# Kernel tuning notes

Hardware: AMD Instinct MI355X
Metric: run time of the kernel (lower is better)

## Reference

```python
import jax, jax.numpy as jnp
import numpy as np

N_NODES = 50000
N_EDGES = 1600000
IN_CH = 128
HID_CH = 128


def setup_inputs() -> dict:
    key = jax.random.key(0)
    ks = jax.random.split(key, 8)
    node_embed = jax.random.normal(ks[0], (N_NODES, IN_CH), dtype=jnp.float32)
    node_pos = jax.random.normal(ks[1], (N_NODES, 3), dtype=jnp.float32)
    edge_index = jax.random.randint(ks[2], (2, N_EDGES), 0, N_NODES, dtype=jnp.int64)
    # Linear weights stored as [in, out] so y = x @ W + b (matches torch x @ W.T + b)
    W_res = jax.random.normal(ks[3], (IN_CH, HID_CH), dtype=jnp.float32) / np.sqrt(IN_CH)
    W_msg = jax.random.normal(ks[4], (2 * IN_CH + 1, HID_CH), dtype=jnp.float32) / np.sqrt(2 * IN_CH + 1)
    b_msg = jax.random.normal(ks[5], (HID_CH,), dtype=jnp.float32) * 0.01
    W_upd = jax.random.normal(ks[6], (IN_CH + HID_CH, HID_CH), dtype=jnp.float32) / np.sqrt(IN_CH + HID_CH)
    b_upd = jax.random.normal(ks[7], (HID_CH,), dtype=jnp.float32) * 0.01
    return {"node_embed": node_embed, "node_pos": node_pos, "edge_index": edge_index,
            "W_res": W_res, "W_msg": W_msg, "b_msg": b_msg, "W_upd": W_upd, "b_upd": b_upd}


def reference(node_embed, node_pos, edge_index, W_res, W_msg, b_msg, W_upd, b_upd):
    row, col = edge_index[0], edge_index[1]
    # squared distance per edge: [E, 1]
    diff = node_pos[row] - node_pos[col]
    dist = jnp.sum(diff * diff, axis=1, keepdims=True)
    # message MLP on concat(src, tgt, dist): [E, 2*in+1] -> [E, hidden]
    msg_in = jnp.concatenate([node_embed[row], node_embed[col], dist], axis=-1)
    msg = jax.nn.relu(msg_in @ W_msg + b_msg)
    # scatter-sum messages into target nodes (index = col, as in original)
    aggr = jax.ops.segment_sum(msg, col, num_segments=N_NODES)
    upd_in = jnp.concatenate([node_embed, aggr], axis=-1)
    new_node_embed = node_embed @ W_res + jax.nn.relu(upd_in @ W_upd + b_upd)
    return new_node_embed
```

## Files before the change

kernel.cpp:

```cpp
#include <hip/hip_runtime.h>
#include <hip/hip_bf16.h>
#include <cstdint>


typedef __bf16 bf16x8 __attribute__((ext_vector_type(8)));
typedef float floatx4 __attribute__((ext_vector_type(4)));
typedef float floatx2 __attribute__((ext_vector_type(2)));
typedef unsigned int uintx4 __attribute__((ext_vector_type(4)));

#define NBINS 1024
#define NCPY 8
#define BINF_CAP 384
#define CAP_OUT 2816
#define CUR_STRIDE 32
#define EPB 8192

__device__ __forceinline__ ushort f2bf(float f) {
  union { float f; uint i; } v; v.f = f;
  uint r = v.i + 0x7fff + ((v.i >> 16) & 1);
  return (ushort)(r >> 16);
}
__device__ __forceinline__ bf16x8 load_frag(const ushort* p) {
  uint4 v = *(const uint4*)p;
  return __builtin_bit_cast(bf16x8, v);
}
__device__ __forceinline__ floatx2 pmax0(floatx2 a) {
#if __has_builtin(__builtin_elementwise_max)
  return __builtin_elementwise_max(a, (floatx2)(0.f));
#else
  floatx2 r; r.x = fmaxf(a.x, 0.f); r.y = fmaxf(a.y, 0.f); return r;
#endif
}
__device__ __forceinline__ floatx2 cvtpk2(uint qu) {
#if __has_builtin(__builtin_amdgcn_cvt_pk_f32_fp8)
  return __builtin_amdgcn_cvt_pk_f32_fp8((int)qu, false);
#else
  floatx2 o = {__builtin_amdgcn_cvt_f32_fp8((int)qu, 0),
               __builtin_amdgcn_cvt_f32_fp8((int)qu, 1)};
  return o;
#endif
}

struct WSrc { const float* s[5]; };

__global__ __launch_bounds__(256) void k01_cast_bin(
    const float* __restrict__ embed, ushort* __restrict__ Eb, int n4, int nb_cast,
    WSrc ws, ushort* __restrict__ Wt,
    const int* __restrict__ ei, int E,
    uint* __restrict__ bin_cursor, uint* __restrict__ binned, int bb)
{
  __shared__ uint hist[NBINS];
  __shared__ uint sbase[NBINS];
  __shared__ uint lcur[NBINS];

  if ((int)blockIdx.x >= bb) {
    int cb = blockIdx.x - bb;
    if (cb < nb_cast) {
      int base = cb * 2048 + threadIdx.x;
#pragma unroll
      for (int k = 0; k < 8; ++k) {
        int i = base + k * 256;
        if (i < n4) {
          float4 v = ((const float4*)embed)[i];
          ushort4 o;
          o.x = f2bf(v.x); o.y = f2bf(v.y); o.z = f2bf(v.z); o.w = f2bf(v.w);
          ((ushort4*)Eb)[i] = o;
        }
      }
      return;
    }
    int wb = cb - nb_cast;
    const float* s = ws.s[wb];
    ushort* d = Wt + wb * 16384;
    for (int i = threadIdx.x; i < 16384; i += 256) {
      int k = i >> 7, n = i & 127;
      d[n * 128 + k] = f2bf(s[i]);
    }
    return;
  }

  const int t = threadIdx.x;
#pragma unroll
  for (int k = 0; k < NBINS / 256; ++k) hist[t + k * 256] = 0;
  __syncthreads();

  const int blk0 = blockIdx.x * EPB;
#pragma unroll
  for (int c = 0; c < EPB / 2048; ++c) {
    int e0 = blk0 + c * 2048 + t * 8;
    if (e0 < E) {
      int4 c0 = ((const int4*)(ei + E + e0))[0];
      int4 c1 = ((const int4*)(ei + E + e0))[1];
      int cc[8];
      cc[0]=c0.x; cc[1]=c0.y; cc[2]=c0.z; cc[3]=c0.w;
      cc[4]=c1.x; cc[5]=c1.y; cc[6]=c1.z; cc[7]=c1.w;
#pragma unroll
      for (int j = 0; j < 8; ++j)
        if (e0 + j < E) atomicAdd(&hist[cc[j] >> 6], 1u);
    }
  }
  __syncthreads();

  const int cpy = blockIdx.x & 7;
  uint* cur = bin_cursor + (size_t)cpy * NBINS * CUR_STRIDE;
#pragma unroll
  for (int k = 0; k < NBINS / 256; ++k) {
    int b2 = t + k * 256;
    uint h = hist[b2];
    sbase[b2] = h ? atomicAdd(cur + (size_t)b2 * CUR_STRIDE, h) : 0u;
    lcur[b2] = 0;
  }
  __syncthreads();

  uint* mybin = binned + (size_t)cpy * NBINS * BINF_CAP;
#pragma unroll
  for (int c = 0; c < EPB / 2048; ++c) {
    int e0 = blk0 + c * 2048 + t * 8;
    if (e0 < E) {
      int4 r0 = ((const int4*)(ei + e0))[0];
      int4 r1 = ((const int4*)(ei + e0))[1];
      int4 c0 = ((const int4*)(ei + E + e0))[0];
      int4 c1 = ((const int4*)(ei + E + e0))[1];
      int rr[8], cc[8];
      rr[0]=r0.x; rr[1]=r0.y; rr[2]=r0.z; rr[3]=r0.w;
      rr[4]=r1.x; rr[5]=r1.y; rr[6]=r1.z; rr[7]=r1.w;
      cc[0]=c0.x; cc[1]=c0.y; cc[2]=c0.z; cc[3]=c0.w;
      cc[4]=c1.x; cc[5]=c1.y; cc[6]=c1.z; cc[7]=c1.w;
#pragma unroll
      for (int j = 0; j < 8; ++j) {
        if (e0 + j < E) {
          int b = cc[j] >> 6;
          uint ofs = atomicAdd(&lcur[b], 1u);
          uint idx = sbase[b] + ofs;
          if (idx < BINF_CAP)
            mybin[(size_t)b * BINF_CAP + idx] = ((uint)cc[j] << 16) | (uint)rr[j];
        }
      }
    }
  }
}

__global__ __launch_bounds__(256) void k2_proj_sort(
    const ushort* __restrict__ Ab, int M, int rt,
    const ushort* __restrict__ W1t, const ushort* __restrict__ W2t,
    const float* __restrict__ b_msg, const float* __restrict__ pos,
    unsigned char* __restrict__ P1, ushort* __restrict__ P2b,
    const uint* __restrict__ bin_cursor, const uint* __restrict__ binned,
    uint* __restrict__ sorted, int* __restrict__ nstart, int* __restrict__ ncnt)
{
  __shared__ ushort sdist[NCPY * BINF_CAP];
  __shared__ uint   srt[CAP_OUT];
  __shared__ float  spos[64 * 3];
  __shared__ uint   h64[64], st64[64], lc64[64];
  __shared__ uint   ccnt[NCPY];
  __shared__ uint   stot;

  if ((int)blockIdx.x >= rt) {
    const int bin = blockIdx.x - rt;
    const int col0 = bin * 64;
    const int ncol = min(64, M - col0);
    const int tid = threadIdx.x;

    if (tid < 64) { h64[tid] = 0; lc64[tid] = 0; }
    if (tid < NCPY)
      ccnt[tid] = min(bin_cursor[((size_t)tid * NBINS + bin) * CUR_STRIDE],
                      (uint)BINF_CAP);
    for (int i = tid; i < ncol * 3; i += 256) spos[i] = pos[(size_t)col0 * 3 + i];
    __syncthreads();

    for (int c = 0; c < NCPY; ++c) {
      const int cnt = (int)ccnt[c];
      const uint* src = binned + ((size_t)c * NBINS + bin) * BINF_CAP;
      for (int i = tid; i < cnt; i += 256) {
        uint rc = src[i];
        uint row = rc & 0xffffu, c6 = (rc >> 16) & 63u;
        float dx = spos[c6 * 3 + 0] - pos[(size_t)row * 3 + 0];
        float dy = spos[c6 * 3 + 1] - pos[(size_t)row * 3 + 1];
        float dz = spos[c6 * 3 + 2] - pos[(size_t)row * 3 + 2];
        sdist[c * BINF_CAP + i] = f2bf(dx * dx + dy * dy + dz * dz);
        atomicAdd(&h64[c6], 1u);
      }
    }
    __syncthreads();

    if (tid == 0) {
      uint run = 0;
      for (int c = 0; c < 64; ++c) { st64[c] = run; run += (h64[c] + 3u) & ~3u; }
      stot = min(run, (uint)CAP_OUT);
    }
    __syncthreads();

    for (int c = 0; c < NCPY; ++c) {
      const int cnt = (int)ccnt[c];
      const uint* src = binned + ((size_t)c * NBINS + bin) * BINF_CAP;
      for (int i = tid; i < cnt; i += 256) {
        uint rc = src[i];
        uint c6 = (rc >> 16) & 63u;
        uint p = st64[c6] + atomicAdd(&lc64[c6], 1u);
        if (p < CAP_OUT)
          srt[p] = ((rc & 0xffffu) << 16) | (uint)sdist[c * BINF_CAP + i];
      }
    }
    __syncthreads();

    const size_t obase = (size_t)bin * CAP_OUT;
    for (int i = tid; i < (int)stot; i += 256)
      sorted[obase + i] = srt[i];
    if (tid < ncol) {
      nstart[col0 + tid] = (int)(obase + st64[tid]);
      ncnt[col0 + tid] = (int)h64[tid];
    }
    return;
  }

  const int wv = threadIdx.x >> 6, lane = threadIdx.x & 63;
  const int q = lane >> 4, lr = lane & 15;
  const int m0 = blockIdx.x * 32;
  const int n0 = wv * 32;

  const ushort* Wt2[2] = {W1t, W2t};
  bf16x8 bfr[2][2][4];
#pragma unroll
  for (int ws = 0; ws < 2; ++ws)
#pragma unroll
    for (int nt = 0; nt < 2; ++nt) {
      int colc = n0 + nt * 16 + lr;
#pragma unroll
      for (int kc = 0; kc < 4; ++kc)
        bfr[ws][nt][kc] = load_frag(Wt2[ws] + colc * 128 + kc * 32 + q * 8);
    }

  floatx4 z = {0.f, 0.f, 0.f, 0.f};
  floatx4 acc[2][2][2];
#pragma unroll
  for (int ws = 0; ws < 2; ++ws)
#pragma unroll
    for (int mt = 0; mt < 2; ++mt)
#pragma unroll
      for (int nt = 0; nt < 2; ++nt) acc[ws][mt][nt] = z;

  const int r0 = min(m0 + lr, M - 1);
  const int r1 = min(m0 + 16 + lr, M - 1);
#pragma unroll
  for (int kc = 0; kc < 4; ++kc) {
    bf16x8 a0 = load_frag(Ab + (size_t)r0 * 128 + kc * 32 + q * 8);
    bf16x8 a1 = load_frag(Ab + (size_t)r1 * 128 + kc * 32 + q * 8);
#pragma unroll
    for (int ws = 0; ws < 2; ++ws)
#pragma unroll
      for (int nt = 0; nt < 2; ++nt) {
        acc[ws][0][nt] = __builtin_amdgcn_mfma_f32_16x16x32_bf16(a0, bfr[ws][nt][kc], acc[ws][0][nt], 0, 0, 0);
        acc[ws][1][nt] = __builtin_amdgcn_mfma_f32_16x16x32_bf16(a1, bfr[ws][nt][kc], acc[ws][1][nt], 0, 0, 0);
      }
  }

#pragma unroll
  for (int nt = 0; nt < 2; ++nt) {
    int colc = n0 + nt * 16 + lr;
    float bias = b_msg[colc];
#pragma unroll
    for (int mt = 0; mt < 2; ++mt)
#pragma unroll
      for (int i = 0; i < 4; ++i) {
        int r = m0 + mt * 16 + q * 4 + i;
        if (r < M) {
          int p8 = __builtin_amdgcn_cvt_pk_fp8_f32(acc[0][mt][nt][i], 0.f, 0, false);
          P1[(size_t)r * 128 + colc] = (unsigned char)(p8 & 0xff);
          P2b[(size_t)r * 128 + colc] = f2bf(acc[1][mt][nt][i] + bias);
        }
      }
  }
}

__global__ __launch_bounds__(256) void aggregate(const int* __restrict__ ncnt,
                                                 const int* __restrict__ nstart,
                                                 const uint* __restrict__ sorted,
                                                 const unsigned char* __restrict__ P1,
                                                 const ushort* __restrict__ P2b,
                                                 const float* __restrict__ wd,
                                                 ushort* __restrict__ aggr, int M)
{
  const int lane = threadIdx.x & 63;
  const int ch = lane * 2;
  const int wid = blockIdx.x * 4 + (threadIdx.x >> 6);
  const int nw = gridDim.x * 4;

  float2 wl = *(const float2*)(wd + ch);
  floatx2 wv = {wl.x, wl.y};

  for (int n = wid; n < M; n += nw) {
    uint p2u = *(const uint*)(P2b + (size_t)n * 128 + ch);
    floatx2 p2 = {__int_as_float((int)(p2u << 16)),
                  __int_as_float((int)(p2u & 0xffff0000u))};

    const int cnt = ncnt[n];
    const uint* base = sorted + nstart[n];

    floatx2 accA = {0.f, 0.f}, accB = {0.f, 0.f};

    auto edge = [&](uint rec, floatx2& acc) {
      float d = __int_as_float((int)(rec << 16));
      uint off = ((rec >> 9) & 0x007fff80u) | (uint)ch;
      uint qu = (uint)*(const ushort*)(P1 + off);
#if __has_builtin(__builtin_elementwise_fma)
      floatx2 u = __builtin_elementwise_fma((floatx2)(d), wv, p2);
#else
      floatx2 u = (floatx2)(d) * wv + p2;
#endif
      floatx2 t = cvtpk2(qu) + u;
      acc += pmax0(t);
    };

    int i = 0;
    for (; i + 8 <= cnt; i += 8) {
      uintx4 ra = __builtin_nontemporal_load((const uintx4*)(base + i));
      uintx4 rb = __builtin_nontemporal_load((const uintx4*)(base + i + 4));
      edge(ra.x, accA); edge(ra.y, accB); edge(ra.z, accA); edge(ra.w, accB);
      edge(rb.x, accA); edge(rb.y, accB); edge(rb.z, accA); edge(rb.w, accB);
    }
    for (; i < cnt; ++i) edge(base[i], accA);

    floatx2 acc = accA + accB;
    uint o = (uint)f2bf(acc.x) | ((uint)f2bf(acc.y) << 16);
    *(uint*)(aggr + (size_t)n * 128 + ch) = o;
  }
}

__global__ __launch_bounds__(256) void gemm_upd_mfma(
    const ushort* __restrict__ Eb, const ushort* __restrict__ Gb, int M,
    const ushort* __restrict__ Wu1t, const ushort* __restrict__ Wu2t,
    const ushort* __restrict__ Wrt, const float* __restrict__ b_upd,
    float* __restrict__ out)
{
  const int wv = threadIdx.x >> 6, lane = threadIdx.x & 63;
  const int q = lane >> 4, lr = lane & 15;
  const int m0 = blockIdx.x * 128;
  const int n0 = wv * 32;

  bf16x8 b1[2][4], b2[2][4], br[2][4];
#pragma unroll
  for (int nt = 0; nt < 2; ++nt) {
    int colc = n0 + nt * 16 + lr;
#pragma unroll
    for (int kc = 0; kc < 4; ++kc) {
      b1[nt][kc] = load_frag(Wu1t + colc * 128 + kc * 32 + q * 8);
      b2[nt][kc] = load_frag(Wu2t + colc * 128 + kc * 32 + q * 8);
      br[nt][kc] = load_frag(Wrt  + colc * 128 + kc * 32 + q * 8);
    }
  }

  floatx4 z = {0.f, 0.f, 0.f, 0.f};

  for (int rc = 0; rc < 4; ++rc) {
    const int mb = m0 + rc * 32;
    if (mb >= M) break;

    floatx4 acc_u[2][2], acc_r[2][2];
#pragma unroll
    for (int mt = 0; mt < 2; ++mt)
#pragma unroll
      for (int nt = 0; nt < 2; ++nt) { acc_u[mt][nt] = z; acc_r[mt][nt] = z; }

    const int r0 = min(mb + lr, M - 1);
    const int r1 = min(mb + 16 + lr, M - 1);
#pragma unroll
    for (int kc = 0; kc < 4; ++kc) {
      bf16x8 ae0 = load_frag(Eb + (size_t)r0 * 128 + kc * 32 + q * 8);
      bf16x8 ae1 = load_frag(Eb + (size_t)r1 * 128 + kc * 32 + q * 8);
      bf16x8 ag0 = load_frag(Gb + (size_t)r0 * 128 + kc * 32 + q * 8);
      bf16x8 ag1 = load_frag(Gb + (size_t)r1 * 128 + kc * 32 + q * 8);
#pragma unroll
      for (int nt = 0; nt < 2; ++nt) {
        acc_u[0][nt] = __builtin_amdgcn_mfma_f32_16x16x32_bf16(ae0, b1[nt][kc], acc_u[0][nt], 0, 0, 0);
        acc_u[1][nt] = __builtin_amdgcn_mfma_f32_16x16x32_bf16(ae1, b1[nt][kc], acc_u[1][nt], 0, 0, 0);
        acc_u[0][nt] = __builtin_amdgcn_mfma_f32_16x16x32_bf16(ag0, b2[nt][kc], acc_u[0][nt], 0, 0, 0);
        acc_u[1][nt] = __builtin_amdgcn_mfma_f32_16x16x32_bf16(ag1, b2[nt][kc], acc_u[1][nt], 0, 0, 0);
        acc_r[0][nt] = __builtin_amdgcn_mfma_f32_16x16x32_bf16(ae0, br[nt][kc], acc_r[0][nt], 0, 0, 0);
        acc_r[1][nt] = __builtin_amdgcn_mfma_f32_16x16x32_bf16(ae1, br[nt][kc], acc_r[1][nt], 0, 0, 0);
      }
    }

#pragma unroll
    for (int nt = 0; nt < 2; ++nt) {
      int colc = n0 + nt * 16 + lr;
      float bias = b_upd[colc];
#pragma unroll
      for (int mt = 0; mt < 2; ++mt)
#pragma unroll
        for (int i = 0; i < 4; ++i) {
          int r = mb + mt * 16 + q * 4 + i;
          if (r < M)
            out[(size_t)r * 128 + colc] = acc_r[mt][nt][i] + fmaxf(acc_u[mt][nt][i] + bias, 0.f);
        }
    }
  }
}

extern "C" void kernel_launch(void* const* d_in, const int* in_sizes, int n_in,
                              void* d_out, int out_size, void* d_ws, size_t ws_size,
                              hipStream_t stream)
{
  const float* embed = (const float*)d_in[0];
  const float* pos   = (const float*)d_in[1];
  const int*   ei    = (const int*)d_in[2];
  const float* W_res = (const float*)d_in[3];
  const float* W_msg = (const float*)d_in[4];
  const float* b_msg = (const float*)d_in[5];
  const float* W_upd = (const float*)d_in[6];
  const float* b_upd = (const float*)d_in[7];
  float* out = (float*)d_out;

  const int M = in_sizes[0] / 128;
  const int E = in_sizes[2] / 2;

  ushort* Eb = (ushort*)d_ws;
  unsigned char* P1f8 = (unsigned char*)(Eb + (size_t)M * 128);
  ushort* P2b = (ushort*)(P1f8 + (size_t)M * 128);
  ushort* Gb  = P2b + (size_t)M * 128;
  ushort* Wt  = Gb  + (size_t)M * 128;
  uint*   binned = (uint*)(Wt + 5 * 16384);
  uint*   sorted = binned + (size_t)NCPY * NBINS * BINF_CAP;
  int*    nstart = (int*)(sorted + (size_t)NBINS * CAP_OUT);
  int*    ncnt   = nstart + M;
  uint*   bin_cursor = (uint*)(ncnt + M);

  (void)hipMemsetAsync(bin_cursor, 0,
                       (size_t)NCPY * NBINS * CUR_STRIDE * sizeof(uint), stream);

  WSrc wsrc;
  wsrc.s[0] = W_msg;
  wsrc.s[1] = W_msg + 128 * 128;
  wsrc.s[2] = W_res;
  wsrc.s[3] = W_upd;
  wsrc.s[4] = W_upd + 128 * 128;

  int n4 = M * 128 / 4;
  int nb_cast = (n4 + 2047) / 2048;
  int bb = (E + EPB - 1) / EPB;
  k01_cast_bin<<<bb + nb_cast + 5, 256, 0, stream>>>(
      embed, Eb, n4, nb_cast, wsrc, Wt, ei, E, bin_cursor, binned, bb);

  int rt = (M + 31) / 32;
  int nb2 = (M + 63) / 64;
  k2_proj_sort<<<rt + nb2, 256, 0, stream>>>(
      Eb, M, rt, Wt, Wt + 16384, b_msg, pos, P1f8, P2b,
      bin_cursor, binned, sorted, nstart, ncnt);

  int ab = min((M + 3) / 4, 2048);
  aggregate<<<ab, 256, 0, stream>>>(ncnt, nstart, sorted, P1f8, P2b,
                                    W_msg + 256 * 128, Gb, M);

  int rt4 = (M + 127) / 128;
  gemm_upd_mfma<<<rt4, 256, 0, stream>>>(Eb, Gb, M, Wt + 3 * 16384, Wt + 4 * 16384,
                                         Wt + 2 * 16384, b_upd, out);
}
```

Before: 227.9 us.

## Hoist embed-only update and residual GEMMs into projection/sort kernel

Moves the node_embed@W_upd[:128] (with bias) and node_embed@W_res products out of the final kernel and into k2_proj_sort as extra blocks, storing them as bf16 U and R buffers. The final kernel then only does the aggregate GEMM and adds U and R from memory. The aim is to cut the serial tail after aggregation and overlap those GEMMs with the binning/sort blocks. In exchange, U and R add global write and read traffic, and R is now rounded to bf16, which costs some precision.

```diff
diff --git a/kernel.cpp b/kernel.cpp
--- a/kernel.cpp
+++ b/kernel.cpp
@@ -19,6 +19,9 @@
   union { float f; uint i; } v; v.f = f;
   uint r = v.i + 0x7fff + ((v.i >> 16) & 1);
   return (ushort)(r >> 16);
+}
+__device__ __forceinline__ float bf2f(ushort u) {
+  return __int_as_float((int)((uint)u << 16));
 }
 __device__ __forceinline__ bf16x8 load_frag(const ushort* p) {
   uint4 v = *(const uint4*)p;
@@ -141,12 +144,15 @@
 }
 
 __global__ __launch_bounds__(256) void k2_proj_sort(
-    const ushort* __restrict__ Ab, int M, int rt,
+    const ushort* __restrict__ Ab, int M, int rt, int nsrt,
     const ushort* __restrict__ W1t, const ushort* __restrict__ W2t,
-    const float* __restrict__ b_msg, const float* __restrict__ pos,
+    const ushort* __restrict__ Wu1t, const ushort* __restrict__ Wrt,
+    const float* __restrict__ b_msg, const float* __restrict__ b_upd,
+    const float* __restrict__ pos,
     unsigned char* __restrict__ P1, ushort* __restrict__ P2b,
     const uint* __restrict__ bin_cursor, const uint* __restrict__ binned,
-    uint* __restrict__ sorted, int* __restrict__ nstart, int* __restrict__ ncnt)
+    uint* __restrict__ sorted, int* __restrict__ nstart, int* __restrict__ ncnt,
+    ushort* __restrict__ U, ushort* __restrict__ R)
 {
   __shared__ ushort sdist[NCPY * BINF_CAP];
   __shared__ uint   srt[CAP_OUT];
@@ -155,8 +161,9 @@
   __shared__ uint   ccnt[NCPY];
   __shared__ uint   stot;
 
-  if ((int)blockIdx.x >= rt) {
-    const int bin = blockIdx.x - rt;
+  const int bid = (int)blockIdx.x;
+  if (bid >= rt && bid < rt + nsrt) {
+    const int bin = bid - rt;
     const int col0 = bin * 64;
     const int ncol = min(64, M - col0);
     const int tid = threadIdx.x;
@@ -213,12 +220,16 @@
     return;
   }
 
+  const bool up = (bid >= rt);
+  const int m0 = (up ? (bid - rt - nsrt) : bid) * 32;
   const int wv = threadIdx.x >> 6, lane = threadIdx.x & 63;
   const int q = lane >> 4, lr = lane & 15;
-  const int m0 = blockIdx.x * 32;
   const int n0 = wv * 32;
 
-  const ushort* Wt2[2] = {W1t, W2t};
+  const ushort* Wt2[2];
+  if (up) { Wt2[0] = Wu1t; Wt2[1] = Wrt; }
+  else    { Wt2[0] = W1t;  Wt2[1] = W2t; }
+
   bf16x8 bfr[2][2][4];
 #pragma unroll
   for (int ws = 0; ws < 2; ++ws)
@@ -254,21 +265,39 @@
       }
   }
 
-#pragma unroll
-  for (int nt = 0; nt < 2; ++nt) {
-    int colc = n0 + nt * 16 + lr;
-    float bias = b_msg[colc];
-#pragma unroll
-    for (int mt = 0; mt < 2; ++mt)
-#pragma unroll
-      for (int i = 0; i < 4; ++i) {
-        int r = m0 + mt * 16 + q * 4 + i;
-        if (r < M) {
-          int p8 = __builtin_amdgcn_cvt_pk_fp8_f32(acc[0][mt][nt][i], 0.f, 0, false);
-          P1[(size_t)r * 128 + colc] = (unsigned char)(p8 & 0xff);
-          P2b[(size_t)r * 128 + colc] = f2bf(acc[1][mt][nt][i] + bias);
+  if (up) {
+#pragma unroll
+    for (int nt = 0; nt < 2; ++nt) {
+      int colc = n0 + nt * 16 + lr;
+      float bias = b_upd[colc];
+#pragma unroll
+      for (int mt = 0; mt < 2; ++mt)
+#pragma unroll
+        for (int i = 0; i < 4; ++i) {
+          int r = m0 + mt * 16 + q * 4 + i;
+          if (r < M) {
+            U[(size_t)r * 128 + colc] = f2bf(acc[0][mt][nt][i] + bias);
+            R[(size_t)r * 128 + colc] = f2bf(acc[1][mt][nt][i]);
+          }
         }
-      }
+    }
+  } else {
+#pragma unroll
+    for (int nt = 0; nt < 2; ++nt) {
+      int colc = n0 + nt * 16 + lr;
+      float bias = b_msg[colc];
+#pragma unroll
+      for (int mt = 0; mt < 2; ++mt)
+#pragma unroll
+        for (int i = 0; i < 4; ++i) {
+          int r = m0 + mt * 16 + q * 4 + i;
+          if (r < M) {
+            int p8 = __builtin_amdgcn_cvt_pk_fp8_f32(acc[0][mt][nt][i], 0.f, 0, false);
+            P1[(size_t)r * 128 + colc] = (unsigned char)(p8 & 0xff);
+            P2b[(size_t)r * 128 + colc] = f2bf(acc[1][mt][nt][i] + bias);
+          }
+        }
+    }
   }
 }
 
@@ -326,71 +355,63 @@
   }
 }
 
-__global__ __launch_bounds__(256) void gemm_upd_mfma(
-    const ushort* __restrict__ Eb, const ushort* __restrict__ Gb, int M,
-    const ushort* __restrict__ Wu1t, const ushort* __restrict__ Wu2t,
-    const ushort* __restrict__ Wrt, const float* __restrict__ b_upd,
-    float* __restrict__ out)
+__global__ __launch_bounds__(256) void k4_final(
+    const ushort* __restrict__ Gb, const ushort* __restrict__ U,
+    const ushort* __restrict__ R, const ushort* __restrict__ Wu2t,
+    float* __restrict__ out, int M)
 {
   const int wv = threadIdx.x >> 6, lane = threadIdx.x & 63;
   const int q = lane >> 4, lr = lane & 15;
-  const int m0 = blockIdx.x * 128;
+  const int m0 = blockIdx.x * 64;
   const int n0 = wv * 32;
 
-  bf16x8 b1[2][4], b2[2][4], br[2][4];
+  bf16x8 b2[2][4];
 #pragma unroll
   for (int nt = 0; nt < 2; ++nt) {
     int colc = n0 + nt * 16 + lr;
 #pragma unroll
-    for (int kc = 0; kc < 4; ++kc) {
-      b1[nt][kc] = load_frag(Wu1t + colc * 128 + kc * 32 + q * 8);
+    for (int kc = 0; kc < 4; ++kc)
       b2[nt][kc] = load_frag(Wu2t + colc * 128 + kc * 32 + q * 8);
-      br[nt][kc] = load_frag(Wrt  + colc * 128 + kc * 32 + q * 8);
-    }
   }
 
   floatx4 z = {0.f, 0.f, 0.f, 0.f};
 
-  for (int rc = 0; rc < 4; ++rc) {
+  for (int rc = 0; rc < 2; ++rc) {
     const int mb = m0 + rc * 32;
     if (mb >= M) break;
 
-    floatx4 acc_u[2][2], acc_r[2][2];
+    floatx4 acc[2][2];
 #pragma unroll
     for (int mt = 0; mt < 2; ++mt)
 #pragma unroll
-      for (int nt = 0; nt < 2; ++nt) { acc_u[mt][nt] = z; acc_r[mt][nt] = z; }
+      for (int nt = 0; nt < 2; ++nt) acc[mt][nt] = z;
 
     const int r0 = min(mb + lr, M - 1);
     const int r1 = min(mb + 16 + lr, M - 1);
 #pragma unroll
     for (int kc = 0; kc < 4; ++kc) {
-      bf16x8 ae0 = load_frag(Eb + (size_t)r0 * 128 + kc * 32 + q * 8);
-      bf16x8 ae1 = load_frag(Eb + (size_t)r1 * 128 + kc * 32 + q * 8);
       bf16x8 ag0 = load_frag(Gb + (size_t)r0 * 128 + kc * 32 + q * 8);
       bf16x8 ag1 = load_frag(Gb + (size_t)r1 * 128 + kc * 32 + q * 8);
 #pragma unroll
       for (int nt = 0; nt < 2; ++nt) {
-        acc_u[0][nt] = __builtin_amdgcn_mfma_f32_16x16x32_bf16(ae0, b1[nt][kc], acc_u[0][nt], 0, 0, 0);
-        acc_u[1][nt] = __builtin_amdgcn_mfma_f32_16x16x32_bf16(ae1, b1[nt][kc], acc_u[1][nt], 0, 0, 0);
-        acc_u[0][nt] = __builtin_amdgcn_mfma_f32_16x16x32_bf16(ag0, b2[nt][kc], acc_u[0][nt], 0, 0, 0);
-        acc_u[1][nt] = __builtin_amdgcn_mfma_f32_16x16x32_bf16(ag1, b2[nt][kc], acc_u[1][nt], 0, 0, 0);
-        acc_r[0][nt] = __builtin_amdgcn_mfma_f32_16x16x32_bf16(ae0, br[nt][kc], acc_r[0][nt], 0, 0, 0);
-        acc_r[1][nt] = __builtin_amdgcn_mfma_f32_16x16x32_bf16(ae1, br[nt][kc], acc_r[1][nt], 0, 0, 0);
+        acc[0][nt] = __builtin_amdgcn_mfma_f32_16x16x32_bf16(ag0, b2[nt][kc], acc[0][nt], 0, 0, 0);
+        acc[1][nt] = __builtin_amdgcn_mfma_f32_16x16x32_bf16(ag1, b2[nt][kc], acc[1][nt], 0, 0, 0);
       }
     }
 
 #pragma unroll
     for (int nt = 0; nt < 2; ++nt) {
       int colc = n0 + nt * 16 + lr;
-      float bias = b_upd[colc];
 #pragma unroll
       for (int mt = 0; mt < 2; ++mt)
 #pragma unroll
         for (int i = 0; i < 4; ++i) {
           int r = mb + mt * 16 + q * 4 + i;
-          if (r < M)
-            out[(size_t)r * 128 + colc] = acc_r[mt][nt][i] + fmaxf(acc_u[mt][nt][i] + bias, 0.f);
+          if (r < M) {
+            float u  = bf2f(U[(size_t)r * 128 + colc]);
+            float rv = bf2f(R[(size_t)r * 128 + colc]);
+            out[(size_t)r * 128 + colc] = rv + fmaxf(acc[mt][nt][i] + u, 0.f);
+          }
         }
     }
   }
@@ -423,6 +444,8 @@
   int*    nstart = (int*)(sorted + (size_t)NBINS * CAP_OUT);
   int*    ncnt   = nstart + M;
   uint*   bin_cursor = (uint*)(ncnt + M);
+  ushort* U = (ushort*)(bin_cursor + (size_t)NCPY * NBINS * CUR_STRIDE);
+  ushort* R = U + (size_t)M * 128;
 
   (void)hipMemsetAsync(bin_cursor, 0,
                        (size_t)NCPY * NBINS * CUR_STRIDE * sizeof(uint), stream);
@@ -442,15 +465,15 @@
 
   int rt = (M + 31) / 32;
   int nb2 = (M + 63) / 64;
-  k2_proj_sort<<<rt + nb2, 256, 0, stream>>>(
-      Eb, M, rt, Wt, Wt + 16384, b_msg, pos, P1f8, P2b,
-      bin_cursor, binned, sorted, nstart, ncnt);
+  k2_proj_sort<<<rt + nb2 + rt, 256, 0, stream>>>(
+      Eb, M, rt, nb2, Wt, Wt + 16384, Wt + 3 * 16384, Wt + 2 * 16384,
+      b_msg, b_upd, pos, P1f8, P2b,
+      bin_cursor, binned, sorted, nstart, ncnt, U, R);
 
   int ab = min((M + 3) / 4, 2048);
   aggregate<<<ab, 256, 0, stream>>>(ncnt, nstart, sorted, P1f8, P2b,
                                     W_msg + 256 * 128, Gb, M);
 
-  int rt4 = (M + 127) / 128;
-  gemm_upd_mfma<<<rt4, 256, 0, stream>>>(Eb, Gb, M, Wt + 3 * 16384, Wt + 4 * 16384,
-                                         Wt + 2 * 16384, b_upd, out);
-}
+  int fb = (M + 63) / 64;
+  k4_final<<<fb, 256, 0, stream>>>(Gb, U, R, Wt + 4 * 16384, out, M);
+}
```

Measured after the change: 247.4 us. +8.5%, slower.
